# Kernel optimization log

Measured on AMD Instinct MI355X. Metric: run time of the kernel, lower is better.

Reference implementation:

```python
import jax, jax.numpy as jnp
import numpy as np

N = 100_000   # nodes
E = 3_200_000 # edges
F = 13        # input features
H = 64        # hidden dim
G = 512       # graphs in batch
C = 2         # output classes
BN_EPS = 1e-5


def _linear(key, fan_in, fan_out):
    kw, kb = jax.random.split(key)
    bound = 1.0 / np.sqrt(fan_in)
    W = jax.random.uniform(kw, (fan_in, fan_out), jnp.float32, -bound, bound)
    b = jax.random.uniform(kb, (fan_out,), jnp.float32, -bound, bound)
    return W, b


def _conv_params(key, fin, fout):
    k1, k2, k3 = jax.random.split(key, 3)
    W1, b1 = _linear(k1, fin, fout)
    W2, b2 = _linear(k2, fout, fout)
    gamma = jnp.ones((fout,), jnp.float32)
    beta = jnp.zeros((fout,), jnp.float32)
    mean = jax.random.normal(k3, (fout,), jnp.float32) * 0.1
    var = jnp.ones((fout,), jnp.float32)
    return W1, b1, gamma, beta, mean, var, W2, b2


def setup_inputs() -> dict:
    key = jax.random.key(0)
    ks = jax.random.split(key, 10)
    x = jax.random.normal(ks[0], (N, F), jnp.float32)
    src = jax.random.randint(ks[1], (E,), 0, N, jnp.int32)
    dst = jax.random.randint(ks[2], (E,), 0, N, jnp.int32)
    batch = jnp.sort(jax.random.randint(ks[3], (N,), 0, G, jnp.int32))
    inp = {"x": x, "src": src, "dst": dst, "batch": batch}
    for i, name in enumerate(["c1", "c2", "c3"]):
        fin = F if i == 0 else H
        W1, b1, g, be, m, v, W2, b2 = _conv_params(ks[4 + i], fin, H)
        inp.update({f"{name}_W1": W1, f"{name}_b1": b1, f"{name}_g": g,
                    f"{name}_be": be, f"{name}_m": m, f"{name}_v": v,
                    f"{name}_W2": W2, f"{name}_b2": b2})
    inp["fc1_W"], inp["fc1_b"] = _linear(ks[7], 3 * H, 3 * H)
    inp["fc2_W"], inp["fc2_b"] = _linear(ks[8], 3 * H, C)
    return inp


def _mlp(h, W1, b1, g, be, m, v, W2, b2):
    # Linear -> BatchNorm1d (inference, running stats) -> ReLU -> Linear -> ReLU
    h = h @ W1 + b1
    h = (h - m) * jax.lax.rsqrt(v + BN_EPS) * g + be
    h = jax.nn.relu(h)
    return jax.nn.relu(h @ W2 + b2)


def _gin_conv(x, src, dst, mlp_params):
    # GINConv with eps=0: MLP(x + sum_{j->i} x_j) via scatter-add over edges
    agg = jax.ops.segment_sum(x[src], dst, num_segments=N)
    return _mlp(x + agg, *mlp_params)


def reference(x, src, dst, batch,
              c1_W1, c1_b1, c1_g, c1_be, c1_m, c1_v, c1_W2, c1_b2,
              c2_W1, c2_b1, c2_g, c2_be, c2_m, c2_v, c2_W2, c2_b2,
              c3_W1, c3_b1, c3_g, c3_be, c3_m, c3_v, c3_W2, c3_b2,
              fc1_W, fc1_b, fc2_W, fc2_b):
    h1 = jax.nn.relu(_gin_conv(x, src, dst, (c1_W1, c1_b1, c1_g, c1_be, c1_m, c1_v, c1_W2, c1_b2)))
    h2 = jax.nn.relu(_gin_conv(h1, src, dst, (c2_W1, c2_b1, c2_g, c2_be, c2_m, c2_v, c2_W2, c2_b2)))
    h3 = jax.nn.relu(_gin_conv(h2, src, dst, (c3_W1, c3_b1, c3_g, c3_be, c3_m, c3_v, c3_W2, c3_b2)))
    p1 = jax.ops.segment_sum(h1, batch, num_segments=G)
    p2 = jax.ops.segment_sum(h2, batch, num_segments=G)
    p3 = jax.ops.segment_sum(h3, batch, num_segments=G)
    h = jnp.concatenate([p1, p2, p3], axis=1)  # [G, 3H]
    h = jax.nn.relu(h @ fc1_W + fc1_b)
    # Dropout is identity in eval mode
    h = h @ fc2_W + fc2_b
    return jax.nn.log_softmax(h, axis=-1)
```

## Files before the change

kernel.cpp:

```cpp
#include <hip/hip_runtime.h>

#define NNODES 100000
#define NEDGES 3200000
#define NF 13
#define NFP 16
#define NG 512
#define BN_EPS 1e-5f
#define NTILES (NNODES / 16)
#define CAP 72

#define BSH 9
#define NBUCK ((NNODES + 511) / 512)
#define RCAP 18500
#define PTILE 4096
#define NPBLK ((NEDGES + PTILE - 1) / PTILE)

#define NCHUNK ((NNODES + 63) / 64)
#define NPTASK (3 * NCHUNK)

typedef __attribute__((ext_vector_type(8))) short bf16x8;
typedef __attribute__((ext_vector_type(4))) float f32x4;

__device__ __forceinline__ float bf2f(unsigned short u) {
    return __uint_as_float(((unsigned)u) << 16);
}
__device__ __forceinline__ unsigned short f2bf(float f) {
    unsigned u = __float_as_uint(f);
    unsigned r = (u + 0x7FFFu + ((u >> 16) & 1u)) >> 16;
    return (unsigned short)r;
}

__launch_bounds__(256)
__global__ void partition_kernel(const int* __restrict__ src, const int* __restrict__ dst,
                                 int* __restrict__ gcount, int* __restrict__ pairbuf) {
    __shared__ int lhist[NBUCK];
    __shared__ int lbase[NBUCK];
    __shared__ int lpos[NBUCK];
    int t = threadIdx.x;
    int base = blockIdx.x * PTILE;
    int cnt = NEDGES - base; if (cnt > PTILE) cnt = PTILE;

    int v[PTILE / 256], b[PTILE / 256];
#pragma unroll
    for (int j = 0; j < PTILE / 256; ++j) {
        int i = t + j * 256;
        if (i < cnt) {
            int d = __builtin_nontemporal_load(dst + base + i);
            int s = __builtin_nontemporal_load(src + base + i);
            b[j] = d >> BSH;
            v[j] = ((d & 511) << 17) | s;
        } else b[j] = -1;
    }
    if (t < NBUCK) lhist[t] = 0;
    __syncthreads();
#pragma unroll
    for (int j = 0; j < PTILE / 256; ++j)
        if (b[j] >= 0) atomicAdd(&lhist[b[j]], 1);
    __syncthreads();
    if (t < NBUCK) {
        lbase[t] = atomicAdd(&gcount[t], lhist[t]);
        lpos[t] = 0;
    }
    __syncthreads();
#pragma unroll
    for (int j = 0; j < PTILE / 256; ++j) {
        if (b[j] >= 0) {
            int p = atomicAdd(&lpos[b[j]], 1);
            pairbuf[(size_t)b[j] * RCAP + lbase[b[j]] + p] = v[j];
        }
    }
}

__launch_bounds__(512)
__global__ void bucket_scatter_kernel(const int* __restrict__ pairbuf,
                                      const int* __restrict__ gcount,
                                      int* __restrict__ cursor, int* __restrict__ csr) {
    __shared__ int lcnt[512];
    int bk = blockIdx.x;
    int lo = bk << BSH;
    int cnt = gcount[bk];
    if (threadIdx.x < 512) lcnt[threadIdx.x] = 0;
    __syncthreads();
    const int* pb = pairbuf + (size_t)bk * RCAP;
    for (int i = threadIdx.x; i < cnt; i += 512) {
        int p = pb[i];
        int s = p & 0x1FFFF;
        int dl = p >> 17;
        int pos = atomicAdd(&lcnt[dl], 1);
        csr[(size_t)(lo + dl) * CAP + pos] = s;
    }
    __syncthreads();
    int n = lo + threadIdx.x;
    if (threadIdx.x < 512 && n < NNODES) cursor[n] = n * CAP + lcnt[threadIdx.x];
}

__global__ void cvt_x_kernel(const float* __restrict__ x, unsigned short* __restrict__ xbf) {
    const int total = NNODES * NFP;
    int idx = blockIdx.x * blockDim.x + threadIdx.x;
    int stride = gridDim.x * blockDim.x;
    for (int i = idx; i < total; i += stride) {
        int n = i >> 4;
        int f = i & 15;
        xbf[i] = (f < NF) ? f2bf(x[n * NF + f]) : (unsigned short)0;
    }
}

__global__ void build_frags_kernel(const float* __restrict__ w10, const float* __restrict__ w20,
                                   const float* __restrict__ w11, const float* __restrict__ w21,
                                   const float* __restrict__ w12, const float* __restrict__ w22,
                                   unsigned short* __restrict__ wfrag) {
    int tid = blockIdx.x * blockDim.x + threadIdx.x;
    if (tid >= 3072) return;
    int layer = tid >> 10;
    int rem = tid & 1023;
    int mat = rem >> 9;
    int tile = (rem >> 7) & 3;
    int chunk = (rem >> 6) & 1;
    int lane = rem & 63;
    int quad = lane >> 4, n = lane & 15;
    const float* W = (layer == 0) ? (mat ? w20 : w10)
                   : (layer == 1) ? (mat ? w21 : w11)
                                  : (mat ? w22 : w12);
    int K = (layer == 0 && mat == 0) ? NF : 64;
    unsigned short* o = wfrag + ((size_t)tid) * 8;
#pragma unroll
    for (int j = 0; j < 8; ++j) {
        int k = chunk * 32 + quad * 8 + j;
        float val = (k < K) ? W[k * 64 + tile * 16 + n] : 0.f;
        o[j] = f2bf(val);
    }
}

template <int FSTR, int RL, int UNROLL, int PADZ>
__launch_bounds__(256, 8)
__global__ void agg_vec_kernel(const unsigned short* __restrict__ xin,
                               const int* __restrict__ cursor,
                               const int* __restrict__ csr,
                               unsigned short* __restrict__ y) {
    const int EPG = 64 / RL;
    int lane = threadIdx.x & 63;
    int g = lane / RL;
    int r = lane % RL;
    int wave = (blockIdx.x * blockDim.x + threadIdx.x) >> 6;
    int nw = (gridDim.x * blockDim.x) >> 6;

    for (int n = wave; n < NNODES; n += nw) {
        int beg = n * CAP;
        int end = cursor[n];
        float ax = 0.f, ay = 0.f, az = 0.f, aw = 0.f;
        if (g == 0) {
            ushort4 u = *(const ushort4*)&xin[n * FSTR + r * 4];
            ax = bf2f(u.x); ay = bf2f(u.y); az = bf2f(u.z); aw = bf2f(u.w);
        }
        int j = beg;
        const int STEP = UNROLL * EPG;
        for (; j + STEP <= end; j += STEP) {
#pragma unroll
            for (int t = 0; t < UNROLL; ++t) {
                int e = j + t * EPG + g;
                int i0 = csr[e];
                ushort4 u = *(const ushort4*)&xin[i0 * FSTR + r * 4];
                ax += bf2f(u.x); ay += bf2f(u.y); az += bf2f(u.z); aw += bf2f(u.w);
            }
        }
        for (; j < end; j += EPG) {
            int e = j + g;
            if (e < end) {
                int i0 = csr[e];
                ushort4 u = *(const ushort4*)&xin[i0 * FSTR + r * 4];
                ax += bf2f(u.x); ay += bf2f(u.y); az += bf2f(u.z); aw += bf2f(u.w);
            }
        }
#pragma unroll
        for (int m = RL; m < 64; m <<= 1) {
            ax += __shfl_xor(ax, m, 64);
            ay += __shfl_xor(ay, m, 64);
            az += __shfl_xor(az, m, 64);
            aw += __shfl_xor(aw, m, 64);
        }
        if (g == 0) {
            ushort4 o;
            o.x = f2bf(ax); o.y = f2bf(ay); o.z = f2bf(az); o.w = f2bf(aw);
            *(ushort4*)&y[n * 64 + r * 4] = o;
        } else if (PADZ && g == 1) {
            ushort4 o; o.x = 0; o.y = 0; o.z = 0; o.w = 0;
            *(ushort4*)&y[n * 64 + 16 + r * 4] = o;
        }
    }
}

__launch_bounds__(256, 8)
__global__ void agg_vec8_kernel(const unsigned short* __restrict__ xin,
                                const int* __restrict__ cursor,
                                const int* __restrict__ csr,
                                unsigned short* __restrict__ y) {
    int lane = threadIdx.x & 63;
    int g = lane >> 3;
    int r = lane & 7;
    int wave = (blockIdx.x * blockDim.x + threadIdx.x) >> 6;
    int nw = (gridDim.x * blockDim.x) >> 6;

    for (int n = wave; n < NNODES; n += nw) {
        int beg = n * CAP;
        int end = cursor[n];
        float acc[8] = {0.f, 0.f, 0.f, 0.f, 0.f, 0.f, 0.f, 0.f};
        if (g == 0) {
            bf16x8 u = *(const bf16x8*)&xin[(size_t)n * 64 + r * 8];
#pragma unroll
            for (int k = 0; k < 8; ++k) acc[k] = bf2f((unsigned short)u[k]);
        }
        int j = beg;
        for (; j + 16 <= end; j += 16) {
#pragma unroll
            for (int t = 0; t < 2; ++t) {
                int e = j + t * 8 + g;
                int i0 = csr[e];
                bf16x8 u = *(const bf16x8*)&xin[(size_t)i0 * 64 + r * 8];
#pragma unroll
                for (int k = 0; k < 8; ++k) acc[k] += bf2f((unsigned short)u[k]);
            }
        }
        for (; j < end; j += 8) {
            int e = j + g;
            if (e < end) {
                int i0 = csr[e];
                bf16x8 u = *(const bf16x8*)&xin[(size_t)i0 * 64 + r * 8];
#pragma unroll
                for (int k = 0; k < 8; ++k) acc[k] += bf2f((unsigned short)u[k]);
            }
        }
#pragma unroll
        for (int m = 8; m < 64; m <<= 1) {
#pragma unroll
            for (int k = 0; k < 8; ++k) acc[k] += __shfl_xor(acc[k], m, 64);
        }
        if (g == 0) {
            bf16x8 o;
#pragma unroll
            for (int k = 0; k < 8; ++k) o[k] = (short)f2bf(acc[k]);
            *(bf16x8*)&y[(size_t)n * 64 + r * 8] = o;
        }
    }
}

template <int KC1>
__launch_bounds__(256)
__global__ void mlp_mfma_kernel(const unsigned short* __restrict__ ybf,
                                const unsigned short* __restrict__ wfrag,
                                const float* __restrict__ b1, const float* __restrict__ g,
                                const float* __restrict__ be, const float* __restrict__ m,
                                const float* __restrict__ v,  const float* __restrict__ b2,
                                unsigned short* __restrict__ hout) {
    __shared__ __align__(16) unsigned short zs[4][16 * 72];
    int lane = threadIdx.x & 63;
    int wid = threadIdx.x >> 6;
    int quad = lane >> 4;
    int n16 = lane & 15;

    const bf16x8* wf = (const bf16x8*)wfrag;
    bf16x8 w1f[4][2], w2f[4][2];
#pragma unroll
    for (int t = 0; t < 4; ++t) {
#pragma unroll
        for (int c = 0; c < 2; ++c) {
            w1f[t][c] = wf[((0 * 4 + t) * 2 + c) * 64 + lane];
            w2f[t][c] = wf[((1 * 4 + t) * 2 + c) * 64 + lane];
        }
    }
    float scaleF[4], shiftF[4], b2F[4];
#pragma unroll
    for (int t = 0; t < 4; ++t) {
        int f = t * 16 + n16;
        float sc = g[f] * rsqrtf(v[f] + BN_EPS);
        scaleF[t] = sc;
        shiftF[t] = (b1[f] - m[f]) * sc + be[f];
        b2F[t] = b2[f];
    }

    unsigned short* zrow = &zs[wid][0];
    int ntiles = gridDim.x * 4;
    for (int tile = blockIdx.x * 4 + wid; tile < NTILES; tile += ntiles) {
        int nodebase = tile * 16;
        const unsigned short* yrow = ybf + (size_t)(nodebase + n16) * 64 + quad * 8;
        bf16x8 a0 = *(const bf16x8*)yrow;
        bf16x8 a1 = (KC1 == 2) ? *(const bf16x8*)(yrow + 32) : a0;

        f32x4 acc[4];
#pragma unroll
        for (int t = 0; t < 4; ++t) {
            f32x4 z4 = {0.f, 0.f, 0.f, 0.f};
            z4 = __builtin_amdgcn_mfma_f32_16x16x32_bf16(a0, w1f[t][0], z4, 0, 0, 0);
            if (KC1 == 2)
                z4 = __builtin_amdgcn_mfma_f32_16x16x32_bf16(a1, w1f[t][1], z4, 0, 0, 0);
            acc[t] = z4;
        }
#pragma unroll
        for (int t = 0; t < 4; ++t) {
#pragma unroll
            for (int r = 0; r < 4; ++r) {
                float z = fmaxf(fmaf(acc[t][r], scaleF[t], shiftF[t]), 0.f);
                zrow[(quad * 4 + r) * 72 + t * 16 + n16] = f2bf(z);
            }
        }
        __threadfence_block();
        bf16x8 az0 = *(const bf16x8*)&zrow[n16 * 72 + quad * 8];
        bf16x8 az1 = *(const bf16x8*)&zrow[n16 * 72 + 32 + quad * 8];

        f32x4 acc2[4];
#pragma unroll
        for (int t = 0; t < 4; ++t) {
            f32x4 z4 = {0.f, 0.f, 0.f, 0.f};
            z4 = __builtin_amdgcn_mfma_f32_16x16x32_bf16(az0, w2f[t][0], z4, 0, 0, 0);
            z4 = __builtin_amdgcn_mfma_f32_16x16x32_bf16(az1, w2f[t][1], z4, 0, 0, 0);
            acc2[t] = z4;
        }
#pragma unroll
        for (int t = 0; t < 4; ++t) {
#pragma unroll
            for (int r = 0; r < 4; ++r) {
                float h = fmaxf(acc2[t][r] + b2F[t], 0.f);
                hout[(size_t)(nodebase + quad * 4 + r) * 64 + t * 16 + n16] = f2bf(h);
            }
        }
        __threadfence_block();
    }
}

__launch_bounds__(256)
__global__ void pool_kernel(const unsigned short* __restrict__ h1,
                            const unsigned short* __restrict__ h2,
                            const unsigned short* __restrict__ h3,
                            const int* __restrict__ batch,
                            float* __restrict__ pool) {
    int task = blockIdx.x * 4 + (threadIdx.x >> 6);
    if (task >= NPTASK) return;
    int lane = threadIdx.x & 63;
    int layer = task / NCHUNK;
    int c = task - layer * NCHUNK;
    int n0 = c * 64;
    int n1 = n0 + 64; if (n1 > NNODES) n1 = NNODES;
    const unsigned short* hb = (layer == 0) ? h1 : (layer == 1) ? h2 : h3;
    float acc = 0.f;
    int curg = batch[n0];
    for (int n = n0; n < n1; ++n) {
        int gid = batch[n];
        if (gid != curg) {
            atomicAdd(&pool[(size_t)curg * 192 + layer * 64 + lane], acc);
            acc = 0.f;
            curg = gid;
        }
        acc += bf2f(hb[(size_t)n * 64 + lane]);
    }
    atomicAdd(&pool[(size_t)curg * 192 + layer * 64 + lane], acc);
}

__global__ void head_kernel(const float* __restrict__ pool,
                            const float* __restrict__ fc1W, const float* __restrict__ fc1b,
                            const float* __restrict__ fc2W, const float* __restrict__ fc2b,
                            float* __restrict__ out) {
    __shared__ float ps[192];
    __shared__ float hs[192];
    int gi = blockIdx.x;
    int t = threadIdx.x;
    ps[t] = pool[gi * 192 + t];
    __syncthreads();
    float acc = fc1b[t];
#pragma unroll 8
    for (int k = 0; k < 192; ++k) acc = fmaf(ps[k], fc1W[k * 192 + t], acc);
    hs[t] = fmaxf(acc, 0.f);
    __syncthreads();
    if (t == 0) {
        float l0 = fc2b[0], l1 = fc2b[1];
        for (int k = 0; k < 192; ++k) {
            float h = hs[k];
            l0 = fmaf(h, fc2W[k * 2 + 0], l0);
            l1 = fmaf(h, fc2W[k * 2 + 1], l1);
        }
        float mx = fmaxf(l0, l1);
        float lse = mx + logf(expf(l0 - mx) + expf(l1 - mx));
        out[gi * 2 + 0] = l0 - lse;
        out[gi * 2 + 1] = l1 - lse;
    }
}

extern "C" void kernel_launch(void* const* d_in, const int* in_sizes, int n_in,
                              void* d_out, int out_size, void* d_ws, size_t ws_size,
                              hipStream_t stream) {
    const float* x = (const float*)d_in[0];
    const int* src = (const int*)d_in[1];
    const int* dst = (const int*)d_in[2];
    const int* batch = (const int*)d_in[3];
    const float* c1[8];
    const float* c2[8];
    const float* c3[8];
    for (int i = 0; i < 8; ++i) {
        c1[i] = (const float*)d_in[4 + i];
        c2[i] = (const float*)d_in[12 + i];
        c3[i] = (const float*)d_in[20 + i];
    }
    const float* fc1W = (const float*)d_in[28];
    const float* fc1b = (const float*)d_in[29];
    const float* fc2W = (const float*)d_in[30];
    const float* fc2b = (const float*)d_in[31];
    float* out = (float*)d_out;

    unsigned short* base = (unsigned short*)d_ws;
    const size_t NA = (size_t)NNODES * 64;
    unsigned short* ybf = base;
    unsigned short* xbf = ybf + NA;
    unsigned short* h1  = xbf + (size_t)NNODES * NFP;
    unsigned short* h2  = h1 + NA;
    unsigned short* h3  = h2 + NA;
    unsigned short* wfrag = h3 + NA;
    float* pool = (float*)(wfrag + 3 * 8192);
    int* ibase = (int*)(pool + (size_t)NG * 192);
    int* cursor  = ibase;
    int* gcount  = ibase + NNODES;
    int* csr     = gcount + NBUCK;
    int* pairbuf = csr + (size_t)NNODES * CAP + 256;

    hipMemsetAsync(gcount, 0, NBUCK * sizeof(int), stream);
    hipMemsetAsync(pool, 0, (size_t)NG * 192 * sizeof(float), stream);

    cvt_x_kernel<<<2048, 256, 0, stream>>>(x, xbf);
    build_frags_kernel<<<12, 256, 0, stream>>>(c1[0], c1[6], c2[0], c2[6], c3[0], c3[6], wfrag);
    partition_kernel<<<NPBLK, 256, 0, stream>>>(src, dst, gcount, pairbuf);
    bucket_scatter_kernel<<<NBUCK, 512, 0, stream>>>(pairbuf, gcount, cursor, csr);

    const int AGG_BLOCKS = 25000;
    const int MLP_BLOCKS = 1024;

    agg_vec_kernel<NFP, 4, 2, 1><<<AGG_BLOCKS, 256, 0, stream>>>(xbf, cursor, csr, ybf);
    mlp_mfma_kernel<1><<<MLP_BLOCKS, 256, 0, stream>>>(
        ybf, wfrag + 0 * 8192, c1[1], c1[2], c1[3], c1[4], c1[5], c1[7], h1);

    agg_vec8_kernel<<<AGG_BLOCKS, 256, 0, stream>>>(h1, cursor, csr, ybf);
    mlp_mfma_kernel<2><<<MLP_BLOCKS, 256, 0, stream>>>(
        ybf, wfrag + 1 * 8192, c2[1], c2[2], c2[3], c2[4], c2[5], c2[7], h2);

    agg_vec8_kernel<<<AGG_BLOCKS, 256, 0, stream>>>(h2, cursor, csr, ybf);
    mlp_mfma_kernel<2><<<MLP_BLOCKS, 256, 0, stream>>>(
        ybf, wfrag + 2 * 8192, c3[1], c3[2], c3[3], c3[4], c3[5], c3[7], h3);

    pool_kernel<<<(NPTASK + 3) / 4, 256, 0, stream>>>(h1, h2, h3, batch, pool);
    head_kernel<<<NG, 192, 0, stream>>>(pool, fc1W, fc1b, fc2W, fc2b, out);
}
```

Baseline: 407.3 us.

## Halve partition buckets, widen layer-1 gather to 16B loads, deepen unroll

Edge partitioning now uses 256-node buckets instead of 512, which doubles the bucket count and halves per-bucket capacity, so each bucket_scatter block handles fewer edges. The layer-1 aggregation kernel now has each lane pair load a full 16-feature bf16 row with two 16-byte loads, so 32 edges are processed per step instead of 16. The 64-wide aggregation unroll goes from 2 to 4 edges per lane group, and the MLP grid size is raised to 1563 blocks. Together these aim to increase memory-level parallelism in the gathers and balance the CSR build, at the cost of more registers and more shuffle reductions.

```diff
diff --git a/kernel.cpp b/kernel.cpp
--- a/kernel.cpp
+++ b/kernel.cpp
@@ -9,9 +9,9 @@
 #define NTILES (NNODES / 16)
 #define CAP 72
 
-#define BSH 9
-#define NBUCK ((NNODES + 511) / 512)
-#define RCAP 18500
+#define BSH 8
+#define NBUCK ((NNODES + 255) / 256)
+#define RCAP 9200
 #define PTILE 4096
 #define NPBLK ((NEDGES + PTILE - 1) / PTILE)
 
@@ -48,18 +48,18 @@
             int d = __builtin_nontemporal_load(dst + base + i);
             int s = __builtin_nontemporal_load(src + base + i);
             b[j] = d >> BSH;
-            v[j] = ((d & 511) << 17) | s;
+            v[j] = ((d & 255) << 17) | s;
         } else b[j] = -1;
     }
-    if (t < NBUCK) lhist[t] = 0;
+    for (int k = t; k < NBUCK; k += 256) lhist[k] = 0;
     __syncthreads();
 #pragma unroll
     for (int j = 0; j < PTILE / 256; ++j)
         if (b[j] >= 0) atomicAdd(&lhist[b[j]], 1);
     __syncthreads();
-    if (t < NBUCK) {
-        lbase[t] = atomicAdd(&gcount[t], lhist[t]);
-        lpos[t] = 0;
+    for (int k = t; k < NBUCK; k += 256) {
+        lbase[k] = atomicAdd(&gcount[k], lhist[k]);
+        lpos[k] = 0;
     }
     __syncthreads();
 #pragma unroll
@@ -75,11 +75,11 @@
 __global__ void bucket_scatter_kernel(const int* __restrict__ pairbuf,
                                       const int* __restrict__ gcount,
                                       int* __restrict__ cursor, int* __restrict__ csr) {
-    __shared__ int lcnt[512];
+    __shared__ int lcnt[256];
     int bk = blockIdx.x;
     int lo = bk << BSH;
     int cnt = gcount[bk];
-    if (threadIdx.x < 512) lcnt[threadIdx.x] = 0;
+    if (threadIdx.x < 256) lcnt[threadIdx.x] = 0;
     __syncthreads();
     const int* pb = pairbuf + (size_t)bk * RCAP;
     for (int i = threadIdx.x; i < cnt; i += 512) {
@@ -91,7 +91,7 @@
     }
     __syncthreads();
     int n = lo + threadIdx.x;
-    if (threadIdx.x < 512 && n < NNODES) cursor[n] = n * CAP + lcnt[threadIdx.x];
+    if (threadIdx.x < 256 && n < NNODES) cursor[n] = n * CAP + lcnt[threadIdx.x];
 }
 
 __global__ void cvt_x_kernel(const float* __restrict__ x, unsigned short* __restrict__ xbf) {
@@ -131,60 +131,59 @@
     }
 }
 
-template <int FSTR, int RL, int UNROLL, int PADZ>
 __launch_bounds__(256, 8)
-__global__ void agg_vec_kernel(const unsigned short* __restrict__ xin,
-                               const int* __restrict__ cursor,
-                               const int* __restrict__ csr,
-                               unsigned short* __restrict__ y) {
-    const int EPG = 64 / RL;
+__global__ void agg_l1_kernel(const unsigned short* __restrict__ xin,
+                              const int* __restrict__ cursor,
+                              const int* __restrict__ csr,
+                              unsigned short* __restrict__ y) {
     int lane = threadIdx.x & 63;
-    int g = lane / RL;
-    int r = lane % RL;
+    int g = lane >> 1;
+    int r = lane & 1;
     int wave = (blockIdx.x * blockDim.x + threadIdx.x) >> 6;
     int nw = (gridDim.x * blockDim.x) >> 6;
 
     for (int n = wave; n < NNODES; n += nw) {
         int beg = n * CAP;
         int end = cursor[n];
-        float ax = 0.f, ay = 0.f, az = 0.f, aw = 0.f;
+        float acc[8] = {0.f, 0.f, 0.f, 0.f, 0.f, 0.f, 0.f, 0.f};
         if (g == 0) {
-            ushort4 u = *(const ushort4*)&xin[n * FSTR + r * 4];
-            ax = bf2f(u.x); ay = bf2f(u.y); az = bf2f(u.z); aw = bf2f(u.w);
+            bf16x8 u = *(const bf16x8*)&xin[(size_t)n * NFP + r * 8];
+#pragma unroll
+            for (int k = 0; k < 8; ++k) acc[k] = bf2f((unsigned short)u[k]);
         }
         int j = beg;
-        const int STEP = UNROLL * EPG;
-        for (; j + STEP <= end; j += STEP) {
-#pragma unroll
-            for (int t = 0; t < UNROLL; ++t) {
-                int e = j + t * EPG + g;
+        for (; j + 64 <= end; j += 64) {
+#pragma unroll
+            for (int t = 0; t < 2; ++t) {
+                int e = j + t * 32 + g;
                 int i0 = csr[e];
-                ushort4 u = *(const ushort4*)&xin[i0 * FSTR + r * 4];
-                ax += bf2f(u.x); ay += bf2f(u.y); az += bf2f(u.z); aw += bf2f(u.w);
-            }
-        }
-        for (; j < end; j += EPG) {
+                bf16x8 u = *(const bf16x8*)&xin[(size_t)i0 * NFP + r * 8];
+#pragma unroll
+                for (int k = 0; k < 8; ++k) acc[k] += bf2f((unsigned short)u[k]);
+            }
+        }
+        for (; j < end; j += 32) {
             int e = j + g;
             if (e < end) {
                 int i0 = csr[e];
-                ushort4 u = *(const ushort4*)&xin[i0 * FSTR + r * 4];
-                ax += bf2f(u.x); ay += bf2f(u.y); az += bf2f(u.z); aw += bf2f(u.w);
-            }
-        }
-#pragma unroll
-        for (int m = RL; m < 64; m <<= 1) {
-            ax += __shfl_xor(ax, m, 64);
-            ay += __shfl_xor(ay, m, 64);
-            az += __shfl_xor(az, m, 64);
-            aw += __shfl_xor(aw, m, 64);
+                bf16x8 u = *(const bf16x8*)&xin[(size_t)i0 * NFP + r * 8];
+#pragma unroll
+                for (int k = 0; k < 8; ++k) acc[k] += bf2f((unsigned short)u[k]);
+            }
+        }
+#pragma unroll
+        for (int m = 2; m < 64; m <<= 1) {
+#pragma unroll
+            for (int k = 0; k < 8; ++k) acc[k] += __shfl_xor(acc[k], m, 64);
         }
         if (g == 0) {
-            ushort4 o;
-            o.x = f2bf(ax); o.y = f2bf(ay); o.z = f2bf(az); o.w = f2bf(aw);
-            *(ushort4*)&y[n * 64 + r * 4] = o;
-        } else if (PADZ && g == 1) {
-            ushort4 o; o.x = 0; o.y = 0; o.z = 0; o.w = 0;
-            *(ushort4*)&y[n * 64 + 16 + r * 4] = o;
+            bf16x8 o;
+#pragma unroll
+            for (int k = 0; k < 8; ++k) o[k] = (short)f2bf(acc[k]);
+            *(bf16x8*)&y[(size_t)n * 64 + r * 8] = o;
+        } else if (g == 1) {
+            bf16x8 o = {0, 0, 0, 0, 0, 0, 0, 0};
+            *(bf16x8*)&y[(size_t)n * 64 + 16 + r * 8] = o;
         }
     }
 }
@@ -210,9 +209,9 @@
             for (int k = 0; k < 8; ++k) acc[k] = bf2f((unsigned short)u[k]);
         }
         int j = beg;
-        for (; j + 16 <= end; j += 16) {
-#pragma unroll
-            for (int t = 0; t < 2; ++t) {
+        for (; j + 32 <= end; j += 32) {
+#pragma unroll
+            for (int t = 0; t < 4; ++t) {
                 int e = j + t * 8 + g;
                 int i0 = csr[e];
                 bf16x8 u = *(const bf16x8*)&xin[(size_t)i0 * 64 + r * 8];
@@ -416,7 +415,7 @@
     int* ibase = (int*)(pool + (size_t)NG * 192);
     int* cursor  = ibase;
     int* gcount  = ibase + NNODES;
-    int* csr     = gcount + NBUCK;
+    int* csr     = gcount + NBUCK + 1;
     int* pairbuf = csr + (size_t)NNODES * CAP + 256;
 
     hipMemsetAsync(gcount, 0, NBUCK * sizeof(int), stream);
@@ -428,9 +427,9 @@
     bucket_scatter_kernel<<<NBUCK, 512, 0, stream>>>(pairbuf, gcount, cursor, csr);
 
     const int AGG_BLOCKS = 25000;
-    const int MLP_BLOCKS = 1024;
-
-    agg_vec_kernel<NFP, 4, 2, 1><<<AGG_BLOCKS, 256, 0, stream>>>(xbf, cursor, csr, ybf);
+    const int MLP_BLOCKS = 1563;
+
+    agg_l1_kernel<<<AGG_BLOCKS, 256, 0, stream>>>(xbf, cursor, csr, ybf);
     mlp_mfma_kernel<1><<<MLP_BLOCKS, 256, 0, stream>>>(
         ybf, wfrag + 0 * 8192, c1[1], c1[2], c1[3], c1[4], c1[5], c1[7], h1);
 
```

Measured after the change: 433.2 us. +6.4%, slower.
